# Performance work log

Hardware: AMD Instinct MI355X
Metric: run time of the kernel (lower is better)

Reference implementation:

```python
import jax, jax.numpy as jnp
import numpy as np

H, DM, LQ, LK, DK, DV = 16, 1024, 2048, 2048, 64, 64
B = 2

def setup_inputs() -> dict:
    key = jax.random.key(0)
    ks = jax.random.split(key, 12)
    s = 0.02  # init scale for weights
    return {
        "Q": jax.random.normal(ks[0], (B, LQ, DM), jnp.float32),
        "K": jax.random.normal(ks[1], (B, LK, DM), jnp.float32),
        "V": jax.random.normal(ks[2], (B, LK, DM), jnp.float32),
        "mask": jax.random.randint(ks[3], (B, LQ), 0, 2, jnp.int32),
        "W_Q": jax.random.normal(ks[4], (H * DK, DM), jnp.float32) * s,
        "b_Q": jnp.zeros((H * DK,), jnp.float32),
        "W_K": jax.random.normal(ks[5], (H * DK, DM), jnp.float32) * s,
        "b_K": jnp.zeros((H * DK,), jnp.float32),
        "W_V": jax.random.normal(ks[6], (H * DV, DM), jnp.float32) * s,
        "b_V": jnp.zeros((H * DV,), jnp.float32),
        "W_O": jax.random.normal(ks[7], (DM, H * DV), jnp.float32) * s,
        "b_O": jnp.zeros((DM,), jnp.float32),
    }

def reference(Q, K, V, mask, W_Q, b_Q, W_K, b_K, W_V, b_V, W_O, b_O):
    b = Q.shape[0]
    q = (Q @ W_Q.T + b_Q).reshape(b, LQ, H, DK)
    k = (K @ W_K.T + b_K).reshape(b, LK, H, DK)
    v = (V @ W_V.T + b_V).reshape(b, LK, H, DV)
    # scores: [b, h, q, k]
    A = jnp.einsum('bqhd,bkhd->bhqk', q, k) / jnp.sqrt(jnp.float32(DK))
    # mask masks whole QUERY rows; softmax is over the query axis (dim=1 in torch's [B*h, lq, lk])
    A = jnp.where(mask[:, None, :, None] == 0, -jnp.inf, A)
    alpha = jax.nn.softmax(A, axis=2)  # over query axis, per original masked branch
    out = jnp.einsum('bhqk,bkhd->bqhd', alpha, v).reshape(b, LQ, H * DV)
    return out @ W_O.T + b_O + Q  # output proj + residual
```

## Files before the change

### kernel.cpp

```cpp
#include <hip/hip_runtime.h>
#include <hip/hip_bf16.h>
#include <stdint.h>

using frag8 = __attribute__((ext_vector_type(8))) short;
using f32x4 = __attribute__((ext_vector_type(4))) float;

#define MFMA16 __builtin_amdgcn_mfma_f32_16x16x32_bf16

#if __has_builtin(__builtin_amdgcn_exp2f)
#define EXP2F(x) __builtin_amdgcn_exp2f(x)
#else
#define EXP2F(x) __expf((x) * 0.6931471805599453f)
#endif
#if __has_builtin(__builtin_amdgcn_rcpf)
#define RCPF(x) __builtin_amdgcn_rcpf(x)
#else
#define RCPF(x) (1.0f / (x))
#endif

#define SCALE_Q 0.18033688011112042f

__device__ __forceinline__ short f2bf(float f) {
    union { float f; uint32_t u; } x; x.f = f;
    uint32_t r = x.u + 0x7fffu + ((x.u >> 16) & 1u);
    return (short)(r >> 16);
}
__device__ __forceinline__ float bf2f(short s) {
    union { uint32_t u; float f; } x; x.u = ((uint32_t)(uint16_t)s) << 16;
    return x.f;
}
__device__ __forceinline__ uint32_t pack2bf(float a, float b) {
    float2 t; t.x = a; t.y = b;
    __hip_bfloat162 h = __float22bfloat162_rn(t);
    union { __hip_bfloat162 h; uint32_t u; } c; c.h = h;
    return c.u;
}

__global__ __launch_bounds__(64) void k_compact(const int* __restrict__ mask,
                                                int* __restrict__ idx,
                                                int* __restrict__ nU) {
    const int b = blockIdx.x, ln = threadIdx.x;
    const int* m = mask + b * 2048;
    int* id = idx + b * 2048;
    int base = 0;
    for (int c = 0; c < 32; c++) {
        int i = c * 64 + ln;
        int mv = m[i];
        unsigned long long bal = __ballot(mv != 0);
        int rank = __popcll(bal & ((1ull << ln) - 1ull));
        if (mv) id[base + rank] = i;
        base += __popcll(bal);
    }
    if (ln == 0) nU[b] = base;
    int nUr = (base + 63) & ~63;
    for (int i = base + ln; i < nUr; i += 64) id[i] = 0;
}

__global__ __launch_bounds__(256) void k_zero(uint4* __restrict__ p, int n16) {
    int i = blockIdx.x * 256 + threadIdx.x;
    if (i < n16) { uint4 z = {0, 0, 0, 0}; p[i] = z; }
}

__global__ __launch_bounds__(256) void k_gather(const short* __restrict__ q_s,
                                                const int* __restrict__ idx,
                                                const int* __restrict__ nU,
                                                short* __restrict__ q_c) {
    const int bh = blockIdx.x, tile = blockIdx.y, b = bh >> 4;
    const int n = nU[b], nUr = (n + 63) & ~63;
    const int i = tile * 64 + (threadIdx.x >> 2);
    if (i >= nUr) return;
    const int src = idx[b * 2048 + i];
    const uint4* sp = (const uint4*)(q_s + ((size_t)bh * 2048 + src) * 64);
    uint4* dp = (uint4*)(q_c + ((size_t)bh * 2048 + i) * 64);
    const int c = threadIdx.x & 3;
    dp[c] = sp[c];
    dp[c + 4] = sp[c + 4];
}

__global__ __launch_bounds__(256) void k_cvt_all(
    const float* __restrict__ s0, const float* __restrict__ s1,
    const float* __restrict__ s2, const float* __restrict__ s3,
    const float* __restrict__ s4, const float* __restrict__ s5,
    const float* __restrict__ s6,
    short* __restrict__ d0, short* __restrict__ d1, short* __restrict__ d2,
    short* __restrict__ d3, short* __restrict__ d4, short* __restrict__ d5,
    short* __restrict__ d6) {
    const int A4 = 1048576, W4 = 262144;
    int i = blockIdx.x * 256 + threadIdx.x;
    int st = gridDim.x * 256;
    const int total = 3 * A4 + 4 * W4;
    for (; i < total; i += st) {
        const float* s; short* d; int j;
        if (i < A4)            { s = s0; d = d0; j = i; }
        else if (i < 2 * A4)   { s = s1; d = d1; j = i - A4; }
        else if (i < 3 * A4)   { s = s2; d = d2; j = i - 2 * A4; }
        else {
            int t = i - 3 * A4; int seg = t / W4; j = t - seg * W4;
            s = seg == 0 ? s3 : seg == 1 ? s4 : seg == 2 ? s5 : s6;
            d = seg == 0 ? d3 : seg == 1 ? d4 : seg == 2 ? d5 : d6;
        }
        float4 v = reinterpret_cast<const float4*>(s)[j];
        ushort4 o;
        o.x = (uint16_t)f2bf(v.x); o.y = (uint16_t)f2bf(v.y);
        o.z = (uint16_t)f2bf(v.z); o.w = (uint16_t)f2bf(v.w);
        reinterpret_cast<ushort4*>(d)[j] = o;
    }
}

__device__ __forceinline__ void stage64x128(const short* __restrict__ g, int rs,
                                            short* lds, int tid) {
#pragma unroll
    for (int j = 0; j < 2; j++) {
        int chunk = j * 256 + tid;
        int row = chunk >> 3, c = chunk & 7;
        int sc = c ^ (row & 7);
        __builtin_amdgcn_global_load_lds(
            (const __attribute__((address_space(1))) uint32_t*)(g + (size_t)row * rs + sc * 8),
            (__attribute__((address_space(3))) uint32_t*)(lds + (j * 256 + (tid & 192)) * 8),
            16, 0, 0);
    }
}
__device__ __forceinline__ frag8 ldswz(const short* lds, int row, int cc) {
    return *(const frag8*)(lds + row * 64 + ((cc ^ (row & 7)) << 3));
}

__device__ __forceinline__ void stage_tiles(const short* __restrict__ As,
                                            const short* __restrict__ Bs,
                                            short* lA, short* lB,
                                            int w, int ln) {
#pragma unroll
    for (int j = 0; j < 2; j++) {
        int cb = (w * 2 + j) * 64;
        int c  = cb + ln;
        int row = c >> 2, c8 = c & 3;
        __builtin_amdgcn_global_load_lds(
            (const __attribute__((address_space(1))) uint32_t*)(As + row * 1024 + c8 * 8),
            (__attribute__((address_space(3))) uint32_t*)(lA + cb * 8), 16, 0, 0);
        __builtin_amdgcn_global_load_lds(
            (const __attribute__((address_space(1))) uint32_t*)(Bs + row * 1024 + c8 * 8),
            (__attribute__((address_space(3))) uint32_t*)(lB + cb * 8), 16, 0, 0);
    }
}

__global__ __launch_bounds__(256) void k_proj3(const short* __restrict__ A0,
                                               const short* __restrict__ A1,
                                               const short* __restrict__ A2,
                                               const short* __restrict__ B0,
                                               const short* __restrict__ B1,
                                               const short* __restrict__ B2,
                                               const float* __restrict__ bias0,
                                               const float* __restrict__ bias1,
                                               const float* __restrict__ bias2,
                                               short* __restrict__ dst0,
                                               short* __restrict__ dst1,
                                               short* __restrict__ dst2) {
    __shared__ short lA[2][4096];
    __shared__ short lB[2][4096];
    const int z = blockIdx.z;
    const short* A  = z == 0 ? A0 : z == 1 ? A1 : A2;
    const short* Bt = z == 0 ? B0 : z == 1 ? B1 : B2;
    const float* bias = z == 0 ? bias0 : z == 1 ? bias1 : bias2;
    short* dst = z == 0 ? dst0 : z == 1 ? dst1 : dst2;
    const float scale = z == 0 ? SCALE_Q : 1.0f;

    const int tid = threadIdx.x, w = tid >> 6, ln = tid & 63;
    const int wm = w >> 1, wn = w & 1, r16 = ln & 15, g = ln >> 4;
    const int tn = blockIdx.x * 128, tm = blockIdx.y * 128;
    const short* Ab = A + (size_t)tm * 1024;
    const short* Bb = Bt + (size_t)tn * 1024;

    f32x4 acc[4][4] = {};
    stage_tiles(Ab, Bb, &lA[0][0], &lB[0][0], w, ln);
    int buf = 0;
    for (int ks = 0; ks < 32; ks++) {
        __syncthreads();
        if (ks + 1 < 32)
            stage_tiles(Ab + (ks + 1) * 32, Bb + (ks + 1) * 32,
                        &lA[buf ^ 1][0], &lB[buf ^ 1][0], w, ln);
        frag8 af[4], bg[4];
#pragma unroll
        for (int mf = 0; mf < 4; mf++)
            af[mf] = *(const frag8*)&lA[buf][(wm * 64 + mf * 16 + r16) * 32 + g * 8];
#pragma unroll
        for (int nf = 0; nf < 4; nf++)
            bg[nf] = *(const frag8*)&lB[buf][(wn * 64 + nf * 16 + r16) * 32 + g * 8];
#pragma unroll
        for (int mf = 0; mf < 4; mf++)
#pragma unroll
            for (int nf = 0; nf < 4; nf++)
                acc[mf][nf] = MFMA16(af[mf], bg[nf], acc[mf][nf], 0, 0, 0);
        buf ^= 1;
    }
#pragma unroll
    for (int mf = 0; mf < 4; mf++)
#pragma unroll
        for (int nf = 0; nf < 4; nf++)
#pragma unroll
            for (int r = 0; r < 4; r++) {
                int m = tm + wm * 64 + mf * 16 + g * 4 + r;
                int n = tn + wn * 64 + nf * 16 + r16;
                float val = (acc[mf][nf][r] + bias[n]) * scale;
                int b = m >> 11, seq = m & 2047, h = n >> 6, d = n & 63;
                dst[((size_t)(b * 16 + h) * 2048 + seq) * 64 + d] = f2bf(val);
            }
}

__global__ __launch_bounds__(256, 4) void k_stats(const short* __restrict__ k_s,
                                                  const short* __restrict__ q_c,
                                                  const int* __restrict__ nU,
                                                  const short* __restrict__ v_s,
                                                  short* __restrict__ vhatT) {
    __shared__ short lQ[2][4096];
    __shared__ float lD[64];
    __shared__ short lT[64 * 70];
    const int wg = blockIdx.x;
    const int lin = (wg & 7) * 128 + (wg >> 3);
    const int bh = lin >> 5, kt = lin & 31;
    const int b = bh >> 4;
    const int n = nU[b], nUr = (n + 63) & ~63;
    const int tid = threadIdx.x, w = tid >> 6, ln = tid & 63;
    const int r16 = ln & 15, g = ln >> 4;
    const int kbase = kt * 64 + w * 16;

    const short* kp = k_s + ((size_t)bh * 2048 + kbase) * 64;
    frag8 kf[2];
#pragma unroll
    for (int kk = 0; kk < 2; kk++)
        kf[kk] = *(const frag8*)(kp + r16 * 64 + kk * 32 + g * 8);

    const short* qsp = q_c + (size_t)bh * 2048 * 64;
    float dacc[4] = {};
    const f32x4 z4 = {0.f, 0.f, 0.f, 0.f};

    if (nUr > 0) {
        stage64x128(qsp, 64, &lQ[0][0], tid);
        int buf = 0;
        for (int qb = 0; qb < nUr; qb += 64) {
            __syncthreads();
            if (qb + 64 < nUr)
                stage64x128(qsp + (size_t)(qb + 64) * 64, 64, &lQ[buf ^ 1][0], tid);
            const short* Qc = &lQ[buf][0];
#pragma unroll
            for (int nf = 0; nf < 4; nf++) {
                float fm = (qb + nf * 16 + r16 < n) ? 1.0f : 0.0f;
                frag8 bq0 = ldswz(Qc, nf * 16 + r16, g);
                frag8 bq1 = ldswz(Qc, nf * 16 + r16, 4 + g);
                f32x4 s = MFMA16(kf[0], bq0, z4, 0, 0, 0);
                s = MFMA16(kf[1], bq1, s, 0, 0, 0);
#pragma unroll
                for (int r = 0; r < 4; r++)
                    dacc[r] += fm * EXP2F(s[r]);
            }
            buf ^= 1;
        }
    }
#pragma unroll
    for (int r = 0; r < 4; r++) {
        float v = dacc[r];
#pragma unroll
        for (int off = 1; off < 16; off <<= 1)
            v += __shfl_xor(v, off, 16);
        dacc[r] = v;
    }
    if (r16 == 0) {
#pragma unroll
        for (int r = 0; r < 4; r++)
            lD[w * 16 + g * 4 + r] = RCPF(dacc[r]);
    }
    const short* vrow = v_s + ((size_t)bh * 2048 + kt * 64) * 64;
#pragma unroll
    for (int i = 0; i < 4; i++) {
        int idx4 = i * 256 + tid;
        int row = idx4 >> 4, c4 = idx4 & 15;
        uint2 u = *(const uint2*)(vrow + (size_t)row * 64 + c4 * 4);
        *(uint32_t*)&lT[row * 70 + c4 * 4]     = u.x;
        *(uint32_t*)&lT[row * 70 + c4 * 4 + 2] = u.y;
    }
    __syncthreads();
    {
        int d = tid >> 2, kc = tid & 3;
        short* dstp = vhatT + ((size_t)bh * 64 + d) * 2048 + kt * 64 + kc * 16;
        uint32_t wd[8];
#pragma unroll
        for (int j2 = 0; j2 < 8; j2++) {
            int k0 = kc * 16 + j2 * 2;
            float v0 = bf2f(lT[k0 * 70 + d]) * lD[k0];
            float v1 = bf2f(lT[(k0 + 1) * 70 + d]) * lD[k0 + 1];
            wd[j2] = pack2bf(v0, v1);
        }
        uint4 o0 = {wd[0], wd[1], wd[2], wd[3]};
        uint4 o1 = {wd[4], wd[5], wd[6], wd[7]};
        *(uint4*)dstp = o0;
        *((uint4*)dstp + 1) = o1;
    }
}

__global__ __launch_bounds__(256, 4) void k_apply(const short* __restrict__ q_c,
                                                  const short* __restrict__ k_s,
                                                  const short* __restrict__ vhatT,
                                                  const int* __restrict__ idx,
                                                  const int* __restrict__ nU,
                                                  short* __restrict__ attn) {
    __shared__ short lK[2][4096];
    __shared__ short lV[2][4096];
    __shared__ short lP[64 * 64];
    const int wg = blockIdx.x;
    const int lin = (wg & 7) * 128 + (wg >> 3);
    const int bh = lin >> 5, qt = lin & 31;
    const int b = bh >> 4, h = bh & 15;
    const int n = nU[b];
    if (qt * 64 >= n) return;
    const int tid = threadIdx.x, w = tid >> 6, ln = tid & 63;
    const int r16 = ln & 15, g = ln >> 4;

    const short* qp = q_c + ((size_t)bh * 2048 + qt * 64 + w * 16) * 64;
    frag8 qf[2];
#pragma unroll
    for (int kk = 0; kk < 2; kk++)
        qf[kk] = *(const frag8*)(qp + r16 * 64 + kk * 32 + g * 8);

    const short* kp = k_s + (size_t)bh * 2048 * 64;
    const short* vp = vhatT + (size_t)bh * 64 * 2048;

    f32x4 oacc[4] = {};
    const f32x4 z4 = {0.f, 0.f, 0.f, 0.f};
    const int prow = w * 16 + r16, rx = prow & 7;

    stage64x128(kp, 64, &lK[0][0], tid);
    stage64x128(vp, 2048, &lV[0][0], tid);
    int buf = 0;
    for (int kb = 0; kb < 2048; kb += 64) {
        __syncthreads();
        if (kb + 64 < 2048) {
            stage64x128(kp + (size_t)(kb + 64) * 64, 64, &lK[buf ^ 1][0], tid);
            stage64x128(vp + kb + 64, 2048, &lV[buf ^ 1][0], tid);
        }
        const short* Kc = &lK[buf][0];
        const short* Vc = &lV[buf][0];
#pragma unroll
        for (int mf2 = 0; mf2 < 4; mf2++) {
            f32x4 s = z4;
#pragma unroll
            for (int kk = 0; kk < 2; kk++)
                s = MFMA16(ldswz(Kc, mf2 * 16 + r16, kk * 4 + g), qf[kk], s, 0, 0, 0);
            float e0 = EXP2F(s[0]), e1 = EXP2F(s[1]);
            float e2 = EXP2F(s[2]), e3 = EXP2F(s[3]);
            uint2 pk;
            pk.x = pack2bf(e0, e1);
            pk.y = pack2bf(e2, e3);
            int o = mf2 * 32 + g * 8;
            int addr = prow * 128 + (((o >> 4) ^ rx) << 4) + (o & 15);
            *(uint2*)((char*)lP + addr) = pk;
        }
        frag8 pa[2];
#pragma unroll
        for (int kk = 0; kk < 2; kk++)
            pa[kk] = *(const frag8*)((char*)lP + prow * 128 + (((kk * 4 + g) ^ rx) << 4));
#pragma unroll
        for (int nf = 0; nf < 4; nf++)
#pragma unroll
            for (int kk = 0; kk < 2; kk++)
                oacc[nf] = MFMA16(pa[kk], ldswz(Vc, nf * 16 + r16, kk * 4 + g), oacc[nf], 0, 0, 0);
        buf ^= 1;
    }
#pragma unroll
    for (int r = 0; r < 4; r++) {
        int lq = qt * 64 + w * 16 + g * 4 + r;
        if (lq < n) {
            int qg = idx[b * 2048 + lq];
#pragma unroll
            for (int nf = 0; nf < 4; nf++) {
                int d = nf * 16 + r16;
                attn[((size_t)(b * 2048 + qg)) * 1024 + h * 64 + d] = f2bf(oacc[nf][r]);
            }
        }
    }
}

__global__ __launch_bounds__(256) void k_final(const short* __restrict__ A,
                                               const short* __restrict__ Bt,
                                               const float* __restrict__ bias,
                                               const float* __restrict__ Qres,
                                               float* __restrict__ out) {
    __shared__ short lA[2][4096];
    __shared__ short lB[2][4096];
    const int tid = threadIdx.x, w = tid >> 6, ln = tid & 63;
    const int wm = w >> 1, wn = w & 1, r16 = ln & 15, g = ln >> 4;
    const int tn = blockIdx.x * 128, tm = blockIdx.y * 128;
    const short* Ab = A + (size_t)tm * 1024;
    const short* Bb = Bt + (size_t)tn * 1024;

    f32x4 acc[4][4] = {};
    stage_tiles(Ab, Bb, &lA[0][0], &lB[0][0], w, ln);
    int buf = 0;
    for (int ks = 0; ks < 32; ks++) {
        __syncthreads();
        if (ks + 1 < 32)
            stage_tiles(Ab + (ks + 1) * 32, Bb + (ks + 1) * 32,
                        &lA[buf ^ 1][0], &lB[buf ^ 1][0], w, ln);
        frag8 af[4], bg[4];
#pragma unroll
        for (int mf = 0; mf < 4; mf++)
            af[mf] = *(const frag8*)&lA[buf][(wm * 64 + mf * 16 + r16) * 32 + g * 8];
#pragma unroll
        for (int nf = 0; nf < 4; nf++)
            bg[nf] = *(const frag8*)&lB[buf][(wn * 64 + nf * 16 + r16) * 32 + g * 8];
#pragma unroll
        for (int mf = 0; mf < 4; mf++)
#pragma unroll
            for (int nf = 0; nf < 4; nf++)
                acc[mf][nf] = MFMA16(af[mf], bg[nf], acc[mf][nf], 0, 0, 0);
        buf ^= 1;
    }
#pragma unroll
    for (int mf = 0; mf < 4; mf++)
#pragma unroll
        for (int nf = 0; nf < 4; nf++)
#pragma unroll
            for (int r = 0; r < 4; r++) {
                int m = tm + wm * 64 + mf * 16 + g * 4 + r;
                int n = tn + wn * 64 + nf * 16 + r16;
                float val = acc[mf][nf][r] + bias[n] + Qres[(size_t)m * 1024 + n];
                out[(size_t)m * 1024 + n] = val;
            }
}

extern "C" void kernel_launch(void* const* d_in, const int* in_sizes, int n_in,
                              void* d_out, int out_size, void* d_ws, size_t ws_size,
                              hipStream_t stream) {
    (void)in_sizes; (void)n_in; (void)out_size; (void)ws_size;
    const float* Qf  = (const float*)d_in[0];
    const float* Kf  = (const float*)d_in[1];
    const float* Vf  = (const float*)d_in[2];
    const int*   msk = (const int*)d_in[3];
    const float* WQ  = (const float*)d_in[4];
    const float* bQ  = (const float*)d_in[5];
    const float* WK  = (const float*)d_in[6];
    const float* bK  = (const float*)d_in[7];
    const float* WV  = (const float*)d_in[8];
    const float* bV  = (const float*)d_in[9];
    const float* WO  = (const float*)d_in[10];
    const float* bO  = (const float*)d_in[11];
    float* out = (float*)d_out;

    char* p = (char*)d_ws;
    const size_t SZ_ACT = (size_t)4096 * 1024 * 2;
    const size_t SZ_W   = (size_t)1024 * 1024 * 2;
    short* Qb  = (short*)p; p += SZ_ACT;
    short* Kb  = (short*)p; p += SZ_ACT;
    short* Vb  = (short*)p; p += SZ_ACT;
    short* Wqb = (short*)p; p += SZ_W;
    short* Wkb = (short*)p; p += SZ_W;
    short* Wvb = (short*)p; p += SZ_W;
    short* Wob = (short*)p; p += SZ_W;
    short* q_s = (short*)p; p += SZ_ACT;
    short* k_s = (short*)p; p += SZ_ACT;
    short* v_s = (short*)p; p += SZ_ACT;
    int* idx = (int*)p; p += (size_t)2 * 2048 * 4;
    int* nU  = (int*)p; p += 64;
    short* vhatT = Kb;
    short* attn  = Qb;
    short* q_c   = Vb;

    k_compact<<<2, 64, 0, stream>>>(msk, idx, nU);

    k_cvt_all<<<4096, 256, 0, stream>>>(Qf, Kf, Vf, WQ, WK, WV, WO,
                                        Qb, Kb, Vb, Wqb, Wkb, Wvb, Wob);

    k_proj3<<<dim3(8, 32, 3), 256, 0, stream>>>(Qb, Kb, Vb, Wqb, Wkb, Wvb,
                                                bQ, bK, bV, q_s, k_s, v_s);

    k_gather<<<dim3(32, 32), 256, 0, stream>>>(q_s, idx, nU, q_c);

    k_stats<<<1024, 256, 0, stream>>>(k_s, q_c, nU, v_s, vhatT);

    k_zero<<<2048, 256, 0, stream>>>((uint4*)attn, 4096 * 1024 * 2 / 16);

    k_apply<<<1024, 256, 0, stream>>>(q_c, k_s, vhatT, idx, nU, attn);

    k_final<<<dim3(8, 32), 256, 0, stream>>>(attn, Wob, bO, Qf, out);
}
```

Baseline: 177.9 us.

## Fuse activation fp32->bf16 conversion into projection GEMM and split attention key range

```diff
diff --git a/kernel.cpp b/kernel.cpp
--- a/kernel.cpp
+++ b/kernel.cpp
@@ -34,6 +34,21 @@
     __hip_bfloat162 h = __float22bfloat162_rn(t);
     union { __hip_bfloat162 h; uint32_t u; } c; c.h = h;
     return c.u;
+}
+__device__ __forceinline__ frag8 cvt8(float4 a, float4 b) {
+    frag8 r;
+    r[0] = f2bf(a.x); r[1] = f2bf(a.y); r[2] = f2bf(a.z); r[3] = f2bf(a.w);
+    r[4] = f2bf(b.x); r[5] = f2bf(b.y); r[6] = f2bf(b.z); r[7] = f2bf(b.w);
+    return r;
+}
+__device__ __forceinline__ frag8 addbf8(uint4 x, uint4 y) {
+    frag8 r;
+    const ushort* xs = (const ushort*)&x;
+    const ushort* ys = (const ushort*)&y;
+#pragma unroll
+    for (int i = 0; i < 8; i++)
+        r[i] = f2bf(bf2f((short)xs[i]) + bf2f((short)ys[i]));
+    return r;
 }
 
 __global__ __launch_bounds__(64) void k_compact(const int* __restrict__ mask,
@@ -56,9 +71,22 @@
     for (int i = base + ln; i < nUr; i += 64) id[i] = 0;
 }
 
-__global__ __launch_bounds__(256) void k_zero(uint4* __restrict__ p, int n16) {
+__global__ __launch_bounds__(256) void k_zero2(uint4* __restrict__ a,
+                                               uint4* __restrict__ b, int n16) {
     int i = blockIdx.x * 256 + threadIdx.x;
-    if (i < n16) { uint4 z = {0, 0, 0, 0}; p[i] = z; }
+    if (i < n16) { uint4 z = {0, 0, 0, 0}; a[i] = z; b[i] = z; }
+}
+
+__global__ __launch_bounds__(256) void k_psum(short* __restrict__ p0,
+                                              const short* __restrict__ p1, int n8) {
+    int i = blockIdx.x * 256 + threadIdx.x;
+    int st = gridDim.x * 256;
+    for (; i < n8; i += st) {
+        uint4 a = ((const uint4*)p0)[i];
+        uint4 b = ((const uint4*)p1)[i];
+        frag8 r = addbf8(a, b);
+        ((uint4*)p0)[i] = *(uint4*)&r;
+    }
 }
 
 __global__ __launch_bounds__(256) void k_gather(const short* __restrict__ q_s,
@@ -77,33 +105,23 @@
     dp[c + 4] = sp[c + 4];
 }
 
-__global__ __launch_bounds__(256) void k_cvt_all(
+__global__ __launch_bounds__(256) void k_cvt_w(
     const float* __restrict__ s0, const float* __restrict__ s1,
     const float* __restrict__ s2, const float* __restrict__ s3,
-    const float* __restrict__ s4, const float* __restrict__ s5,
-    const float* __restrict__ s6,
-    short* __restrict__ d0, short* __restrict__ d1, short* __restrict__ d2,
-    short* __restrict__ d3, short* __restrict__ d4, short* __restrict__ d5,
-    short* __restrict__ d6) {
-    const int A4 = 1048576, W4 = 262144;
+    short* __restrict__ d0, short* __restrict__ d1,
+    short* __restrict__ d2, short* __restrict__ d3) {
+    const int W4 = 262144;
     int i = blockIdx.x * 256 + threadIdx.x;
     int st = gridDim.x * 256;
-    const int total = 3 * A4 + 4 * W4;
-    for (; i < total; i += st) {
-        const float* s; short* d; int j;
-        if (i < A4)            { s = s0; d = d0; j = i; }
-        else if (i < 2 * A4)   { s = s1; d = d1; j = i - A4; }
-        else if (i < 3 * A4)   { s = s2; d = d2; j = i - 2 * A4; }
-        else {
-            int t = i - 3 * A4; int seg = t / W4; j = t - seg * W4;
-            s = seg == 0 ? s3 : seg == 1 ? s4 : seg == 2 ? s5 : s6;
-            d = seg == 0 ? d3 : seg == 1 ? d4 : seg == 2 ? d5 : d6;
-        }
-        float4 v = reinterpret_cast<const float4*>(s)[j];
+    for (; i < 4 * W4; i += st) {
+        int seg = i / W4, j = i - seg * W4;
+        const float* sp = seg == 0 ? s0 : seg == 1 ? s1 : seg == 2 ? s2 : s3;
+        short* dp = seg == 0 ? d0 : seg == 1 ? d1 : seg == 2 ? d2 : d3;
+        float4 v = ((const float4*)sp)[j];
         ushort4 o;
         o.x = (uint16_t)f2bf(v.x); o.y = (uint16_t)f2bf(v.y);
         o.z = (uint16_t)f2bf(v.z); o.w = (uint16_t)f2bf(v.w);
-        reinterpret_cast<ushort4*>(d)[j] = o;
+        ((ushort4*)dp)[j] = o;
     }
 }
 
@@ -141,23 +159,28 @@
             (__attribute__((address_space(3))) uint32_t*)(lB + cb * 8), 16, 0, 0);
     }
 }
-
-__global__ __launch_bounds__(256) void k_proj3(const short* __restrict__ A0,
-                                               const short* __restrict__ A1,
-                                               const short* __restrict__ A2,
-                                               const short* __restrict__ B0,
-                                               const short* __restrict__ B1,
-                                               const short* __restrict__ B2,
-                                               const float* __restrict__ bias0,
-                                               const float* __restrict__ bias1,
-                                               const float* __restrict__ bias2,
-                                               short* __restrict__ dst0,
-                                               short* __restrict__ dst1,
-                                               short* __restrict__ dst2) {
+__device__ __forceinline__ void stage_b(const short* __restrict__ Bs,
+                                        short* lB, int w, int ln) {
+#pragma unroll
+    for (int j = 0; j < 2; j++) {
+        int cb = (w * 2 + j) * 64;
+        int c  = cb + ln;
+        int row = c >> 2, c8 = c & 3;
+        __builtin_amdgcn_global_load_lds(
+            (const __attribute__((address_space(1))) uint32_t*)(Bs + row * 1024 + c8 * 8),
+            (__attribute__((address_space(3))) uint32_t*)(lB + cb * 8), 16, 0, 0);
+    }
+}
+
+__global__ __launch_bounds__(256) void k_proj3(
+    const float* __restrict__ A0, const float* __restrict__ A1, const float* __restrict__ A2,
+    const short* __restrict__ B0, const short* __restrict__ B1, const short* __restrict__ B2,
+    const float* __restrict__ bias0, const float* __restrict__ bias1, const float* __restrict__ bias2,
+    short* __restrict__ dst0, short* __restrict__ dst1, short* __restrict__ dst2) {
     __shared__ short lA[2][4096];
     __shared__ short lB[2][4096];
     const int z = blockIdx.z;
-    const short* A  = z == 0 ? A0 : z == 1 ? A1 : A2;
+    const float* A  = z == 0 ? A0 : z == 1 ? A1 : A2;
     const short* Bt = z == 0 ? B0 : z == 1 ? B1 : B2;
     const float* bias = z == 0 ? bias0 : z == 1 ? bias1 : bias2;
     short* dst = z == 0 ? dst0 : z == 1 ? dst1 : dst2;
@@ -166,17 +189,36 @@
     const int tid = threadIdx.x, w = tid >> 6, ln = tid & 63;
     const int wm = w >> 1, wn = w & 1, r16 = ln & 15, g = ln >> 4;
     const int tn = blockIdx.x * 128, tm = blockIdx.y * 128;
-    const short* Ab = A + (size_t)tm * 1024;
+    const float* Ab = A + (size_t)tm * 1024;
     const short* Bb = Bt + (size_t)tn * 1024;
 
+    const int cb0 = (w * 2 + 0) * 64 + ln, cb1 = (w * 2 + 1) * 64 + ln;
+    const int rA0 = cb0 >> 2, cA0 = cb0 & 3, rA1 = cb1 >> 2, cA1 = cb1 & 3;
+
+    float4 ra[4];
     f32x4 acc[4][4] = {};
-    stage_tiles(Ab, Bb, &lA[0][0], &lB[0][0], w, ln);
+
+    {
+        const float* a0 = Ab + (size_t)rA0 * 1024 + cA0 * 8;
+        ra[0] = *(const float4*)a0; ra[1] = *(const float4*)(a0 + 4);
+        const float* a1 = Ab + (size_t)rA1 * 1024 + cA1 * 8;
+        ra[2] = *(const float4*)a1; ra[3] = *(const float4*)(a1 + 4);
+    }
+    stage_b(Bb, &lB[0][0], w, ln);
+    *(frag8*)&lA[0][cb0 * 8] = cvt8(ra[0], ra[1]);
+    *(frag8*)&lA[0][cb1 * 8] = cvt8(ra[2], ra[3]);
+
     int buf = 0;
     for (int ks = 0; ks < 32; ks++) {
+        if (ks + 1 < 32) {
+            const float* a0 = Ab + (size_t)rA0 * 1024 + (ks + 1) * 32 + cA0 * 8;
+            ra[0] = *(const float4*)a0; ra[1] = *(const float4*)(a0 + 4);
+            const float* a1 = Ab + (size_t)rA1 * 1024 + (ks + 1) * 32 + cA1 * 8;
+            ra[2] = *(const float4*)a1; ra[3] = *(const float4*)(a1 + 4);
+        }
         __syncthreads();
         if (ks + 1 < 32)
-            stage_tiles(Ab + (ks + 1) * 32, Bb + (ks + 1) * 32,
-                        &lA[buf ^ 1][0], &lB[buf ^ 1][0], w, ln);
+            stage_b(Bb + (ks + 1) * 32, &lB[buf ^ 1][0], w, ln);
         frag8 af[4], bg[4];
 #pragma unroll
         for (int mf = 0; mf < 4; mf++)
@@ -189,6 +231,10 @@
 #pragma unroll
             for (int nf = 0; nf < 4; nf++)
                 acc[mf][nf] = MFMA16(af[mf], bg[nf], acc[mf][nf], 0, 0, 0);
+        if (ks + 1 < 32) {
+            *(frag8*)&lA[buf ^ 1][cb0 * 8] = cvt8(ra[0], ra[1]);
+            *(frag8*)&lA[buf ^ 1][cb1 * 8] = cvt8(ra[2], ra[3]);
+        }
         buf ^= 1;
     }
 #pragma unroll
@@ -300,13 +346,14 @@
                                                   const short* __restrict__ vhatT,
                                                   const int* __restrict__ idx,
                                                   const int* __restrict__ nU,
-                                                  short* __restrict__ attn) {
+                                                  short* __restrict__ p0,
+                                                  short* __restrict__ p1) {
     __shared__ short lK[2][4096];
     __shared__ short lV[2][4096];
     __shared__ short lP[64 * 64];
     const int wg = blockIdx.x;
-    const int lin = (wg & 7) * 128 + (wg >> 3);
-    const int bh = lin >> 5, qt = lin & 31;
+    const int lin = (wg & 7) * 256 + (wg >> 3);
+    const int bh = lin >> 6, rem = lin & 63, qt = rem >> 1, sp = rem & 1;
     const int b = bh >> 4, h = bh & 15;
     const int n = nU[b];
     if (qt * 64 >= n) return;
@@ -319,8 +366,8 @@
     for (int kk = 0; kk < 2; kk++)
         qf[kk] = *(const frag8*)(qp + r16 * 64 + kk * 32 + g * 8);
 
-    const short* kp = k_s + (size_t)bh * 2048 * 64;
-    const short* vp = vhatT + (size_t)bh * 64 * 2048;
+    const short* kp = k_s + ((size_t)bh * 2048 + sp * 1024) * 64;
+    const short* vp = vhatT + (size_t)bh * 64 * 2048 + sp * 1024;
 
     f32x4 oacc[4] = {};
     const f32x4 z4 = {0.f, 0.f, 0.f, 0.f};
@@ -329,14 +376,20 @@
     stage64x128(kp, 64, &lK[0][0], tid);
     stage64x128(vp, 2048, &lV[0][0], tid);
     int buf = 0;
-    for (int kb = 0; kb < 2048; kb += 64) {
+    for (int kb = 0; kb < 1024; kb += 64) {
         __syncthreads();
-        if (kb + 64 < 2048) {
+        if (kb + 64 < 1024) {
             stage64x128(kp + (size_t)(kb + 64) * 64, 64, &lK[buf ^ 1][0], tid);
             stage64x128(vp + kb + 64, 2048, &lV[buf ^ 1][0], tid);
         }
         const short* Kc = &lK[buf][0];
         const short* Vc = &lV[buf][0];
+        frag8 vb[4][2];
+#pragma unroll
+        for (int nf = 0; nf < 4; nf++)
+#pragma unroll
+            for (int kk = 0; kk < 2; kk++)
+                vb[nf][kk] = ldswz(Vc, nf * 16 + r16, kk * 4 + g);
 #pragma unroll
         for (int mf2 = 0; mf2 < 4; mf2++) {
             f32x4 s = z4;
@@ -360,9 +413,10 @@
         for (int nf = 0; nf < 4; nf++)
 #pragma unroll
             for (int kk = 0; kk < 2; kk++)
-                oacc[nf] = MFMA16(pa[kk], ldswz(Vc, nf * 16 + r16, kk * 4 + g), oacc[nf], 0, 0, 0);
+                oacc[nf] = MFMA16(pa[kk], vb[nf][kk], oacc[nf], 0, 0, 0);
         buf ^= 1;
     }
+    short* op = sp ? p1 : p0;
 #pragma unroll
     for (int r = 0; r < 4; r++) {
         int lq = qt * 64 + w * 16 + g * 4 + r;
@@ -371,7 +425,7 @@
 #pragma unroll
             for (int nf = 0; nf < 4; nf++) {
                 int d = nf * 16 + r16;
-                attn[((size_t)(b * 2048 + qg)) * 1024 + h * 64 + d] = f2bf(oacc[nf][r]);
+                op[((size_t)(b * 2048 + qg)) * 1024 + h * 64 + d] = f2bf(oacc[nf][r]);
             }
         }
     }
@@ -446,37 +500,36 @@
     char* p = (char*)d_ws;
     const size_t SZ_ACT = (size_t)4096 * 1024 * 2;
     const size_t SZ_W   = (size_t)1024 * 1024 * 2;
-    short* Qb  = (short*)p; p += SZ_ACT;
-    short* Kb  = (short*)p; p += SZ_ACT;
-    short* Vb  = (short*)p; p += SZ_ACT;
+    short* q_s   = (short*)p; p += SZ_ACT;
+    short* k_s   = (short*)p; p += SZ_ACT;
+    short* v_s   = (short*)p; p += SZ_ACT;
+    short* vhatT = (short*)p; p += SZ_ACT;
+    short* p0    = (short*)p; p += SZ_ACT;
+    short* q_c   = (short*)p; p += SZ_ACT;
     short* Wqb = (short*)p; p += SZ_W;
     short* Wkb = (short*)p; p += SZ_W;
     short* Wvb = (short*)p; p += SZ_W;
     short* Wob = (short*)p; p += SZ_W;
-    short* q_s = (short*)p; p += SZ_ACT;
-    short* k_s = (short*)p; p += SZ_ACT;
-    short* v_s = (short*)p; p += SZ_ACT;
     int* idx = (int*)p; p += (size_t)2 * 2048 * 4;
-    int* nU  = (int*)p; p += 64;
-    short* vhatT = Kb;
-    short* attn  = Qb;
-    short* q_c   = Vb;
+    int* nU  = (int*)p; p += 256;
+    short* p1 = v_s;
 
     k_compact<<<2, 64, 0, stream>>>(msk, idx, nU);
 
-    k_cvt_all<<<4096, 256, 0, stream>>>(Qf, Kf, Vf, WQ, WK, WV, WO,
-                                        Qb, Kb, Vb, Wqb, Wkb, Wvb, Wob);
-
-    k_proj3<<<dim3(8, 32, 3), 256, 0, stream>>>(Qb, Kb, Vb, Wqb, Wkb, Wvb,
+    k_cvt_w<<<1024, 256, 0, stream>>>(WQ, WK, WV, WO, Wqb, Wkb, Wvb, Wob);
+
+    k_proj3<<<dim3(8, 32, 3), 256, 0, stream>>>(Qf, Kf, Vf, Wqb, Wkb, Wvb,
                                                 bQ, bK, bV, q_s, k_s, v_s);
 
     k_gather<<<dim3(32, 32), 256, 0, stream>>>(q_s, idx, nU, q_c);
 
     k_stats<<<1024, 256, 0, stream>>>(k_s, q_c, nU, v_s, vhatT);
 
-    k_zero<<<2048, 256, 0, stream>>>((uint4*)attn, 4096 * 1024 * 2 / 16);
-
-    k_apply<<<1024, 256, 0, stream>>>(q_c, k_s, vhatT, idx, nU, attn);
-
-    k_final<<<dim3(8, 32), 256, 0, stream>>>(attn, Wob, bO, Qf, out);
-}
+    k_zero2<<<2048, 256, 0, stream>>>((uint4*)p0, (uint4*)p1, 524288);
+
+    k_apply<<<2048, 256, 0, stream>>>(q_c, k_s, vhatT, idx, nU, p0, p1);
+
+    k_psum<<<2048, 256, 0, stream>>>(p0, p1, 524288);
+
+    k_final<<<dim3(8, 32), 256, 0, stream>>>(p0, Wob, bO, Qf, out);
+}
```

New measurement: 182.8 us. 1.03x slower.
